# Kernel optimization log

Measured on AMD Instinct MI355X. Metric: run time of the kernel, lower is better.

Reference implementation:

```python
import jax, jax.numpy as jnp
import numpy as np

N_NODES = 100000
N_EDGES = 1600000
IN_DIM = 128
HID_DIM = 128
N_MASK = 5000
N_CLASSES = 4


def gcn_layer(x, src, dst, edge_weight, W, b):
    """PyG GCNConv: x' = D^{-1/2} (A + I) D^{-1/2} (x W) + b, with edge weights."""
    n = x.shape[0]
    loop = jnp.arange(n, dtype=src.dtype)
    s = jnp.concatenate([src, loop])                      # [E+N]
    d = jnp.concatenate([dst, loop])                      # [E+N]
    w = jnp.concatenate([edge_weight, jnp.ones((n,), edge_weight.dtype)])
    deg = jax.ops.segment_sum(w, d, num_segments=n)       # weighted in-degree incl. self-loop
    dis = jnp.where(deg > 0, jax.lax.rsqrt(deg), 0.0)     # deg^{-1/2}, inf -> 0
    norm = dis[s] * w * dis[d]                            # [E+N]
    h = x @ W                                             # [N, H] small GEMM
    msg = h[s] * norm[:, None]                            # gather + scale  [E+N, H]
    out = jax.ops.segment_sum(msg, d, num_segments=n)     # scatter-add     [N, H]
    return out + b


def setup_inputs() -> dict:
    key = jax.random.key(0)
    ks = jax.random.split(key, 8)
    x = jax.random.normal(ks[0], (N_NODES, IN_DIM), dtype=jnp.float32)
    edge_weight = jax.random.uniform(ks[1], (N_EDGES,), dtype=jnp.float32)
    W1 = jax.random.normal(ks[2], (IN_DIM, HID_DIM), dtype=jnp.float32) * (1.0 / np.sqrt(IN_DIM))
    b1 = jnp.zeros((HID_DIM,), jnp.float32)
    W2 = jax.random.normal(ks[3], (HID_DIM, HID_DIM), dtype=jnp.float32) * (1.0 / np.sqrt(HID_DIM))
    b2 = jnp.zeros((HID_DIM,), jnp.float32)
    edge_index = jax.random.randint(ks[4], (2, N_EDGES), 0, N_NODES, dtype=jnp.int32)
    mask_idx = jax.random.randint(ks[5], (N_MASK,), 0, N_NODES, dtype=jnp.int32)
    y = jax.random.randint(ks[6], (N_NODES,), 0, N_CLASSES, dtype=jnp.int32)
    return {"x": x, "edge_weight": edge_weight, "W1": W1, "b1": b1,
            "W2": W2, "b2": b2, "edge_index": edge_index,
            "mask_idx": mask_idx, "y": y}


def reference(x, edge_weight, W1, b1, W2, b2, edge_index, mask_idx, y):
    src, dst = edge_index[0], edge_index[1]
    h = gcn_layer(x, src, dst, edge_weight, W1, b1)
    h = jax.nn.relu(h)
    # F.dropout(training=False) in eval mode is identity
    h = gcn_layer(h, src, dst, edge_weight, W2, b2)
    return h[mask_idx], y[mask_idx]
```

## Files before the change

### kernel.cpp

```cpp
#include <hip/hip_runtime.h>

constexpr int N = 100000;
constexpr int E = 1600000;
constexpr int D = 128;
constexpr int M = 5000;

constexpr int MF_BLKS = (N + 255) / 256;

constexpr int NBITS = 7;
constexpr int BUCKET = 1 << NBITS;
constexpr int NB  = (N + BUCKET - 1) / BUCKET;
constexpr int EB  = 2048;
constexpr int NPB = (E + EB - 1) / EB;
constexpr int EBP = 8192;
constexpr int NPP = (E + EBP - 1) / EBP;
constexpr int PREP_BLKS = 32;
constexpr int MB_BLKS = (M + 255) / 256;

typedef __attribute__((ext_vector_type(8))) short bf16x8;
typedef __attribute__((ext_vector_type(4))) float f32x4;


__device__ __forceinline__ unsigned int pack_bf16x2(float a, float b) {
    unsigned int ua = __float_as_uint(a);
    unsigned int ub = __float_as_uint(b);
    ua = (ua + 0x7FFFu + ((ua >> 16) & 1u)) >> 16;
    ub = (ub + 0x7FFFu + ((ub >> 16) & 1u)) & 0xFFFF0000u;
    return ua | ub;
}
__device__ __forceinline__ unsigned short bf16_rne(float a) {
    unsigned int ua = __float_as_uint(a);
    return (unsigned short)((ua + 0x7FFFu + ((ua >> 16) & 1u)) >> 16);
}
__device__ __forceinline__ float bf16_lo(unsigned int u) { return __uint_as_float(u << 16); }
__device__ __forceinline__ float bf16_hi(unsigned int u) { return __uint_as_float(u & 0xFFFF0000u); }


__global__ __launch_bounds__(256) void k_misc1(const int* __restrict__ dst,
                                               int* __restrict__ bucketCnt,
                                               const float* __restrict__ W1,
                                               unsigned int* __restrict__ Wt1,
                                               const int* __restrict__ mask,
                                               unsigned int* __restrict__ maskbit,
                                               unsigned int* __restrict__ needed) {
    __shared__ int h[NB];
    const int t = threadIdx.x;
    if (blockIdx.x < NPB) {
        for (int i = t; i < NB; i += 256) h[i] = 0;
        __syncthreads();
        const int base = blockIdx.x * EB;
#pragma unroll
        for (int i = 0; i < 8; ++i) {
            int e = base + t + i * 256;
            if (e < E) {
                int b = __builtin_nontemporal_load(dst + e) >> NBITS;
                atomicAdd(&h[b], 1);
            }
        }
        __syncthreads();
        for (int i = t; i < NB; i += 256) {
            int c = h[i];
            if (c) atomicAdd(&bucketCnt[i], c);
        }
    } else if (blockIdx.x < NPB + PREP_BLKS) {
        int idx = (blockIdx.x - NPB) * 256 + t;
        int n = idx >> 6, kk = idx & 63;
        float a = W1[(2 * kk) * D + n];
        float b = W1[(2 * kk + 1) * D + n];
        Wt1[idx] = pack_bf16x2(a, b);
    } else {
        int i = (blockIdx.x - NPB - PREP_BLKS) * 256 + t;
        if (i < M) {
            int n = mask[i];
            atomicOr(&maskbit[n >> 5], 1u << (n & 31));
            atomicOr(&needed[n >> 5], 1u << (n & 31));
        }
    }
}


__global__ __launch_bounds__(256) void k_misc2(const int* __restrict__ bucketCnt,
                                               int* __restrict__ bucketBase,
                                               int* __restrict__ gCursor,
                                               const unsigned int* __restrict__ maskbit,
                                               const int* __restrict__ src,
                                               const int* __restrict__ dst,
                                               unsigned int* __restrict__ needed) {
    const int t = threadIdx.x;
    if (blockIdx.x == 0) {
        __shared__ int waveS[4];
        const int lane = t & 63, wave = t >> 6;
        const int idx = t * 4;
        int c[4];
        int s = 0;
#pragma unroll
        for (int g = 0; g < 4; ++g) {
            c[g] = (idx + g < NB) ? bucketCnt[idx + g] : 0;
            s += c[g];
        }
        int v = s;
        for (int off = 1; off < 64; off <<= 1) {
            int u = __shfl_up(v, off);
            if (lane >= off) v += u;
        }
        if (lane == 63) waveS[wave] = v;
        __syncthreads();
        int wb = 0;
        for (int w = 0; w < 4; ++w) if (w < wave) wb += waveS[w];
        int run = wb + v - s;
#pragma unroll
        for (int g = 0; g < 4; ++g) {
            int pos = idx + g;
            if (pos < NB) {
                bucketBase[pos] = run;
                gCursor[pos] = run;
            }
            run += c[g];
        }
        if (t == 255) bucketBase[NB] = E;
    } else {
        const int base = (blockIdx.x - 1) * EB;
#pragma unroll
        for (int i = 0; i < 8; ++i) {
            int e = base + t + i * 256;
            if (e < E) {
                int d = __builtin_nontemporal_load(dst + e);
                if ((maskbit[d >> 5] >> (d & 31)) & 1u) {
                    int s = src[e];
                    atomicOr(&needed[s >> 5], 1u << (s & 31));
                }
            }
        }
    }
}


__global__ __launch_bounds__(1024) void k_part(const int* __restrict__ src,
                                               const int* __restrict__ dst,
                                               const float* __restrict__ ew,
                                               int* __restrict__ gCursor,
                                               unsigned long long* __restrict__ tmp) {
    __shared__ int cnt[NB];
    __shared__ int off[NB];
    __shared__ int rk[NB];
    const int t = threadIdx.x;
    for (int i = t; i < NB; i += 1024) { cnt[i] = 0; rk[i] = 0; }
    __syncthreads();

    const int eb = blockIdx.x * EBP;
    int d_[8], s_[8];
    float w_[8];
#pragma unroll
    for (int i = 0; i < 8; ++i) {
        int e = eb + t + i * 1024;
        if (e < E) {
            d_[i] = __builtin_nontemporal_load(dst + e);
            s_[i] = __builtin_nontemporal_load(src + e);
            w_[i] = __builtin_nontemporal_load(ew + e);
            atomicAdd(&cnt[d_[i] >> NBITS], 1);
        } else {
            d_[i] = -1;
        }
    }
    __syncthreads();

    for (int i = t; i < NB; i += 1024) {
        int c = cnt[i];
        if (c > 0) off[i] = atomicAdd(&gCursor[i], c);
    }
    __syncthreads();

#pragma unroll
    for (int i = 0; i < 8; ++i) {
        if (d_[i] >= 0) {
            int b = d_[i] >> NBITS;
            int r = atomicAdd(&rk[b], 1);
            unsigned long long rec =
                ((unsigned long long)(unsigned int)__float_as_int(w_[i]) << 32) |
                ((unsigned int)s_[i] << NBITS) | (unsigned int)(d_[i] & (BUCKET - 1));
            tmp[(size_t)off[b] + r] = rec;
        }
    }
}


union SMem {
    unsigned int Ws[128 * 68];
    struct { int cnt[BUCKET]; float wsum[BUCKET]; int off[BUCKET]; int waveS[2]; } l;
};


template <bool BF16IN>
__device__ __forceinline__ void gemm_mfma_body(unsigned int* __restrict__ Ws,
                                               const void* __restrict__ Xin,
                                               const unsigned int* __restrict__ Wt,
                                               unsigned short* __restrict__ out, int blk) {
    const int t = threadIdx.x;
#pragma unroll
    for (int i = 0; i < 8; ++i) {
        int f4 = t + i * 256;
        int n = f4 >> 4;
        int k4 = f4 & 15;
        uint4 w = ((const uint4*)Wt)[f4];
        *(uint4*)(&Ws[n * 68 + k4 * 4]) = w;
    }
    __syncthreads();

    const int wv = t >> 6, lane = t & 63;
    const int q = lane >> 4, l15 = lane & 15;
    const int rowBase = blk * 256 + wv * 64;

    f32x4 acc[4][8] = {};
#pragma unroll
    for (int kc = 0; kc < 4; ++kc) {
        bf16x8 af[4];
#pragma unroll
        for (int rt = 0; rt < 4; ++rt) {
            int row = rowBase + rt * 16 + l15;
            if (row > N - 1) row = N - 1;
            union { uint4 u; bf16x8 v; } cv;
            if (BF16IN) {
                cv.u = *(const uint4*)((const unsigned int*)Xin + (size_t)row * 64 + kc * 16 + q * 4);
            } else {
                const float* xr = (const float*)Xin + (size_t)row * D + kc * 32 + q * 8;
                float4 x0 = *(const float4*)xr;
                float4 x1 = *(const float4*)(xr + 4);
                cv.u.x = pack_bf16x2(x0.x, x0.y);
                cv.u.y = pack_bf16x2(x0.z, x0.w);
                cv.u.z = pack_bf16x2(x1.x, x1.y);
                cv.u.w = pack_bf16x2(x1.z, x1.w);
            }
            af[rt] = cv.v;
        }
#pragma unroll
        for (int ct = 0; ct < 8; ++ct) {
            union { uint4 u; bf16x8 v; } bv;
            bv.u = *(const uint4*)(&Ws[(ct * 16 + l15) * 68 + kc * 16 + q * 4]);
#pragma unroll
            for (int rt = 0; rt < 4; ++rt)
                acc[rt][ct] = __builtin_amdgcn_mfma_f32_16x16x32_bf16(af[rt], bv.v, acc[rt][ct], 0, 0, 0);
        }
    }

#pragma unroll
    for (int rt = 0; rt < 4; ++rt) {
#pragma unroll
        for (int ct = 0; ct < 8; ++ct) {
            int col = ct * 16 + l15;
#pragma unroll
            for (int r = 0; r < 4; ++r) {
                int row = rowBase + rt * 16 + q * 4 + r;
                if (row < N) out[(size_t)row * D + col] = bf16_rne(acc[rt][ct][r]);
            }
        }
    }
}


__device__ __forceinline__ void local_a_body(SMem& sm,
                                             const unsigned long long* __restrict__ tmp,
                                             const int* __restrict__ bucketBase,
                                             float* __restrict__ dis,
                                             int* __restrict__ rowStart,
                                             int* __restrict__ offG) {
    const int b = blockIdx.x;
    const int t = threadIdx.x;
    const int segBeg = bucketBase[b];
    const int segEnd = bucketBase[b + 1];

    int*   cnt   = sm.l.cnt;
    float* wsum  = sm.l.wsum;
    int*   waveS = sm.l.waveS;
    if (t < BUCKET) { cnt[t] = 0; wsum[t] = 0.f; }
    __syncthreads();

    for (int e = segBeg + t; e < segEnd; e += 256) {
        unsigned long long rec = tmp[e];
        int dl = (int)(rec & (BUCKET - 1));
        float w = __uint_as_float((unsigned int)(rec >> 32));
        atomicAdd(&cnt[dl], 1);
        atomicAdd(&wsum[dl], w);
    }
    __syncthreads();

    const int lane = t & 63, wv = t >> 6;
    const int pv = (t < BUCKET) ? cnt[t] : 0;
    int v = pv;
    for (int o = 1; o < 64; o <<= 1) {
        int u = __shfl_up(v, o);
        if (lane >= o) v += u;
    }
    if (lane == 63 && wv < 2) waveS[wv] = v;
    __syncthreads();
    if (t < BUCKET) {
        const int wb = (wv == 1) ? waveS[0] : 0;
        const int ex = wb + v - pv;
        offG[b * BUCKET + t] = ex;
        const int node = b * BUCKET + t;
        if (node < N) { rowStart[node] = segBeg + ex; dis[node] = rsqrtf(1.0f + wsum[t]); }
    }
    if (b == NB - 1 && t == 0) rowStart[N] = E;
}


__global__ __launch_bounds__(256) void k_local_g1(const unsigned long long* __restrict__ tmp,
                                                  const int* __restrict__ bucketBase,
                                                  float* __restrict__ dis,
                                                  int* __restrict__ rowStart,
                                                  int* __restrict__ offG,
                                                  const float* __restrict__ x,
                                                  const unsigned int* __restrict__ Wt1,
                                                  unsigned short* __restrict__ A) {
    __shared__ SMem sm;
    if (blockIdx.x < NB) {
        local_a_body(sm, tmp, bucketBase, dis, rowStart, offG);
    } else {
        gemm_mfma_body<false>(sm.Ws, x, Wt1, A, blockIdx.x - NB);
    }
}


__global__ __launch_bounds__(256) void k_local_b(const unsigned long long* __restrict__ tmp,
                                                 const int* __restrict__ bucketBase,
                                                 const int* __restrict__ offG,
                                                 const float* __restrict__ dis,
                                                 int2* __restrict__ pairs) {
    __shared__ int cnt[BUCKET];
    __shared__ int off[BUCKET];
    const int b = blockIdx.x;
    const int t = threadIdx.x;
    if (t < BUCKET) { cnt[t] = 0; off[t] = offG[b * BUCKET + t]; }
    __syncthreads();
    const int segBeg = bucketBase[b];
    const int segEnd = bucketBase[b + 1];
    for (int e = segBeg + t; e < segEnd; e += 256) {
        unsigned long long rec = tmp[e];
        int dl = (int)(rec & (BUCKET - 1));
        int s  = (int)((rec >> NBITS) & 0xFFFFF);
        float w = __uint_as_float((unsigned int)(rec >> 32));
        float v = w * dis[s];
        int r = atomicAdd(&cnt[dl], 1);
        pairs[segBeg + off[dl] + r] = make_int2(s, __float_as_int(v));
    }
}


__global__ __launch_bounds__(256) void k_aggregate(const unsigned int* __restrict__ Hb,
                                                   const int2* __restrict__ pairs,
                                                   const int* __restrict__ rowStart,
                                                   const float* __restrict__ dis,
                                                   const unsigned int* __restrict__ needed,
                                                   const float* __restrict__ b,
                                                   unsigned int* __restrict__ outB) {
    int node = blockIdx.x * 4 + (threadIdx.x >> 6);
    if (node >= N) return;
    if (!((needed[node >> 5] >> (node & 31)) & 1u)) return;
    int lane = threadIdx.x & 63;
    int beg = rowStart[node], end = rowStart[node + 1];

    float ax = 0.f, ay = 0.f;
    int j = beg;
    for (; j + 7 < end; j += 8) {
        int2 p[8];
        unsigned int h[8];
#pragma unroll
        for (int i = 0; i < 8; ++i) p[i] = pairs[j + i];
#pragma unroll
        for (int i = 0; i < 8; ++i) h[i] = Hb[(size_t)p[i].x * 64 + lane];
#pragma unroll
        for (int i = 0; i < 8; ++i) {
            float v = __int_as_float(p[i].y);
            ax += bf16_lo(h[i]) * v;
            ay += bf16_hi(h[i]) * v;
        }
    }
    for (; j + 3 < end; j += 4) {
        int2 p[4];
        unsigned int h[4];
#pragma unroll
        for (int i = 0; i < 4; ++i) p[i] = pairs[j + i];
#pragma unroll
        for (int i = 0; i < 4; ++i) h[i] = Hb[(size_t)p[i].x * 64 + lane];
#pragma unroll
        for (int i = 0; i < 4; ++i) {
            float v = __int_as_float(p[i].y);
            ax += bf16_lo(h[i]) * v;
            ay += bf16_hi(h[i]) * v;
        }
    }
    for (; j < end; ++j) {
        int2 p0 = pairs[j];
        unsigned int h0 = Hb[(size_t)p0.x * 64 + lane];
        float v0 = __int_as_float(p0.y);
        ax += bf16_lo(h0) * v0;
        ay += bf16_hi(h0) * v0;
    }

    float dd = dis[node];
    float sn = dd * dd;
    unsigned int hs = Hb[(size_t)node * 64 + lane];
    float2 bb = ((const float2*)b)[lane];
    float ox = fmaxf(ax * dd + bf16_lo(hs) * sn + bb.x, 0.f);
    float oy = fmaxf(ay * dd + bf16_hi(hs) * sn + bb.y, 0.f);
    __builtin_nontemporal_store(pack_bf16x2(ox, oy), outB + (size_t)node * 64 + lane);
}


__global__ __launch_bounds__(256) void k_agg_mask_B(const unsigned int* __restrict__ Hb,
                                                    const int2* __restrict__ pairs,
                                                    const int* __restrict__ rowStart,
                                                    const float* __restrict__ dis,
                                                    const int* __restrict__ mask,
                                                    const int* __restrict__ y,
                                                    float* __restrict__ aggB,
                                                    float* __restrict__ out) {
    int i = blockIdx.x * 4 + (threadIdx.x >> 6);
    if (i >= M) return;
    int lane = threadIdx.x & 63;
    int node = mask[i];
    int beg = rowStart[node], end = rowStart[node + 1];

    float ax = 0.f, ay = 0.f;
    int j = beg;
    for (; j + 7 < end; j += 8) {
        int2 p[8];
        unsigned int h[8];
#pragma unroll
        for (int ii = 0; ii < 8; ++ii) p[ii] = pairs[j + ii];
#pragma unroll
        for (int ii = 0; ii < 8; ++ii) h[ii] = Hb[(size_t)p[ii].x * 64 + lane];
#pragma unroll
        for (int ii = 0; ii < 8; ++ii) {
            float v = __int_as_float(p[ii].y);
            ax += bf16_lo(h[ii]) * v;
            ay += bf16_hi(h[ii]) * v;
        }
    }
    for (; j < end; ++j) {
        int2 p0 = pairs[j];
        unsigned int h0 = Hb[(size_t)p0.x * 64 + lane];
        float v0 = __int_as_float(p0.y);
        ax += bf16_lo(h0) * v0;
        ay += bf16_hi(h0) * v0;
    }

    float dd = dis[node];
    float sn = dd * dd;
    unsigned int hs = Hb[(size_t)node * 64 + lane];
    float ox = ax * dd + bf16_lo(hs) * sn;
    float oy = ay * dd + bf16_hi(hs) * sn;
    ((float2*)(aggB + (size_t)i * D))[lane] = make_float2(ox, oy);
    if (lane == 0) out[(size_t)M * D + i] = (float)y[node];
}


__global__ __launch_bounds__(256) void k_out_gemm(const float* __restrict__ aggB,
                                                  const float* __restrict__ W2,
                                                  const float* __restrict__ b2,
                                                  float* __restrict__ out) {
    __shared__ float w2s[128 * 132];
    __shared__ float rowL[4][128];
    const int t = threadIdx.x;
    const int wv = t >> 6, lane = t & 63;
    const int row = blockIdx.x * 4 + wv;

    for (int i = t; i < 4096; i += 256) {
        float4 v = ((const float4*)W2)[i];
        int k = (4 * i) >> 7, n = (4 * i) & 127;
        *(float4*)(&w2s[k * 132 + n]) = v;
    }
    float2 a2 = ((const float2*)(aggB + (size_t)row * D))[lane];
    rowL[wv][2 * lane] = a2.x;
    rowL[wv][2 * lane + 1] = a2.y;
    __syncthreads();

    float2 bb = ((const float2*)b2)[lane];
    float acc0 = bb.x, acc1 = bb.y;
#pragma unroll 8
    for (int k = 0; k < 128; ++k) {
        float a = rowL[wv][k];
        float2 w = *(const float2*)(&w2s[k * 132 + 2 * lane]);
        acc0 += a * w.x;
        acc1 += a * w.y;
    }
    ((float2*)(out + (size_t)row * D))[lane] = make_float2(acc0, acc1);
}

extern "C" void kernel_launch(void* const* d_in, const int* in_sizes, int n_in,
                              void* d_out, int out_size, void* d_ws, size_t ws_size,
                              hipStream_t stream) {
    const float* x  = (const float*)d_in[0];
    const float* ew = (const float*)d_in[1];
    const float* W1 = (const float*)d_in[2];
    const float* b1 = (const float*)d_in[3];
    const float* W2 = (const float*)d_in[4];
    const float* b2 = (const float*)d_in[5];
    const int* eidx = (const int*)d_in[6];
    const int* mask = (const int*)d_in[7];
    const int* y    = (const int*)d_in[8];
    const int* src = eidx;
    const int* dst = eidx + E;

    char* ws = (char*)d_ws;
    float* dis      = (float*)(ws);
    int*   rowStart = (int*)(ws + (size_t)512 * 1024);
    unsigned int* maskbit = (unsigned int*)(ws + (size_t)960 * 1024);
    unsigned int* needed  = (unsigned int*)(ws + (size_t)976 * 1024);
    int*   bucketCnt  = (int*)(ws + (size_t)992 * 1024);
    int*   bucketBase = (int*)(ws + (size_t)996 * 1024);
    int*   gCursor    = (int*)(ws + (size_t)1000 * 1024);
    unsigned int* Wt1 = (unsigned int*)(ws + (size_t)1008 * 1024);
    int*   offG     = (int*)(ws + (size_t)1040 * 1024);
    int2*  pairs    = (int2*)(ws + (size_t)2 * 1024 * 1024);
    unsigned long long* tmp = (unsigned long long*)(ws + (size_t)16 * 1024 * 1024);
    unsigned short* A  = (unsigned short*)(ws + (size_t)29 * 1024 * 1024);
    unsigned short* B  = (unsigned short*)(ws + (size_t)55 * 1024 * 1024);
    float* aggB = (float*)(ws + (size_t)81 * 1024 * 1024);

    (void)hipMemsetAsync(ws + (size_t)960 * 1024, 0, (size_t)40 * 1024, stream);
    hipLaunchKernelGGL(k_misc1, dim3(NPB + PREP_BLKS + MB_BLKS), dim3(256), 0, stream,
                       dst, bucketCnt, W1, Wt1, mask, maskbit, needed);

    hipLaunchKernelGGL(k_misc2, dim3(1 + NPB), dim3(256), 0, stream,
                       bucketCnt, bucketBase, gCursor, maskbit, src, dst, needed);

    hipLaunchKernelGGL(k_part, dim3(NPP), dim3(1024), 0, stream,
                       src, dst, ew, gCursor, tmp);

    hipLaunchKernelGGL(k_local_g1, dim3(NB + MF_BLKS), dim3(256), 0, stream,
                       tmp, bucketBase, dis, rowStart, offG, x, Wt1, A);

    hipLaunchKernelGGL(k_local_b, dim3(NB), dim3(256), 0, stream,
                       tmp, bucketBase, offG, dis, pairs);

    hipLaunchKernelGGL(k_aggregate, dim3((N + 3) / 4), dim3(256), 0, stream,
                       (const unsigned int*)A, pairs, rowStart, dis, needed, b1,
                       (unsigned int*)B);

    hipLaunchKernelGGL(k_agg_mask_B, dim3((M + 3) / 4), dim3(256), 0, stream,
                       (const unsigned int*)B, pairs, rowStart, dis, mask, y,
                       aggB, (float*)d_out);
    hipLaunchKernelGGL(k_out_gemm, dim3(M / 4), dim3(256), 0, stream,
                       aggB, W2, b2, (float*)d_out);
}
```

Measured before the change: 287.2 us.

## Fuse bucket-local sort with layer-1 aggregation and mask gather with output GEMM

Merges the per-bucket CSR scatter kernel with the layer-1 aggregation. Each 512-thread block sorts its bucket's edges into shared memory (when the bucket holds at most 3072 edges) and then aggregates its 128 nodes straight from LDS. This avoids re-reading pairs from global memory and drops one launch. The masked second-layer gather is also fused with the W2 GEMM, loading W2 in two halves to limit LDS, which removes the aggB round trip and another launch. The trade-offs are less parallelism in layer-1 aggregation (one block per 128 nodes instead of one wave per node), larger shared memory use, and a reload of W2 in every output block.

After: 276.0 us. 3.9% less time.

```diff
diff --git a/kernel.cpp b/kernel.cpp
--- a/kernel.cpp
+++ b/kernel.cpp
@@ -16,6 +16,7 @@
 constexpr int NPP = (E + EBP - 1) / EBP;
 constexpr int PREP_BLKS = 32;
 constexpr int MB_BLKS = (M + 255) / 256;
+constexpr int CAP = 3072;
 
 typedef __attribute__((ext_vector_type(8))) short bf16x8;
 typedef __attribute__((ext_vector_type(4))) float f32x4;
@@ -186,7 +187,7 @@
 
 union SMem {
     unsigned int Ws[128 * 68];
-    struct { int cnt[BUCKET]; float wsum[BUCKET]; int off[BUCKET]; int waveS[2]; } l;
+    struct { int cnt[BUCKET]; float wsum[BUCKET]; int waveS[2]; } l;
 };
 
 
@@ -261,7 +262,6 @@
                                              const unsigned long long* __restrict__ tmp,
                                              const int* __restrict__ bucketBase,
                                              float* __restrict__ dis,
-                                             int* __restrict__ rowStart,
                                              int* __restrict__ offG) {
     const int b = blockIdx.x;
     const int t = threadIdx.x;
@@ -297,66 +297,154 @@
         const int ex = wb + v - pv;
         offG[b * BUCKET + t] = ex;
         const int node = b * BUCKET + t;
-        if (node < N) { rowStart[node] = segBeg + ex; dis[node] = rsqrtf(1.0f + wsum[t]); }
-    }
-    if (b == NB - 1 && t == 0) rowStart[N] = E;
+        if (node < N) dis[node] = rsqrtf(1.0f + wsum[t]);
+    }
 }
 
 
 __global__ __launch_bounds__(256) void k_local_g1(const unsigned long long* __restrict__ tmp,
                                                   const int* __restrict__ bucketBase,
                                                   float* __restrict__ dis,
-                                                  int* __restrict__ rowStart,
                                                   int* __restrict__ offG,
                                                   const float* __restrict__ x,
                                                   const unsigned int* __restrict__ Wt1,
                                                   unsigned short* __restrict__ A) {
     __shared__ SMem sm;
     if (blockIdx.x < NB) {
-        local_a_body(sm, tmp, bucketBase, dis, rowStart, offG);
+        local_a_body(sm, tmp, bucketBase, dis, offG);
     } else {
         gemm_mfma_body<false>(sm.Ws, x, Wt1, A, blockIdx.x - NB);
     }
 }
 
 
-__global__ __launch_bounds__(256) void k_local_b(const unsigned long long* __restrict__ tmp,
-                                                 const int* __restrict__ bucketBase,
-                                                 const int* __restrict__ offG,
-                                                 const float* __restrict__ dis,
-                                                 int2* __restrict__ pairs) {
+__global__ __launch_bounds__(512) void k_sort_agg(const unsigned long long* __restrict__ tmp,
+                                                  const int* __restrict__ bucketBase,
+                                                  const int* __restrict__ offG,
+                                                  const float* __restrict__ dis,
+                                                  const unsigned int* __restrict__ needed,
+                                                  const float* __restrict__ b,
+                                                  const unsigned int* __restrict__ Hb,
+                                                  int* __restrict__ rowStart,
+                                                  int2* __restrict__ pairs,
+                                                  unsigned int* __restrict__ outB) {
+    __shared__ int2 lp[CAP];
     __shared__ int cnt[BUCKET];
-    __shared__ int off[BUCKET];
-    const int b = blockIdx.x;
-    const int t = threadIdx.x;
-    if (t < BUCKET) { cnt[t] = 0; off[t] = offG[b * BUCKET + t]; }
-    __syncthreads();
-    const int segBeg = bucketBase[b];
-    const int segEnd = bucketBase[b + 1];
-    for (int e = segBeg + t; e < segEnd; e += 256) {
+    __shared__ int offL[BUCKET + 1];
+    const int bk = blockIdx.x;
+    const int t = threadIdx.x;
+    const int segBeg = bucketBase[bk];
+    const int segEnd = bucketBase[bk + 1];
+    const int segLen = segEnd - segBeg;
+    const bool fits = (segLen <= CAP);
+
+    if (t < BUCKET) {
+        int ex = offG[bk * BUCKET + t];
+        offL[t] = ex;
+        cnt[t] = 0;
+        int node = bk * BUCKET + t;
+        if (node < N) rowStart[node] = segBeg + ex;
+    }
+    if (t == 0) offL[BUCKET] = segLen;
+    if (bk == NB - 1 && t == 0) rowStart[N] = E;
+    __syncthreads();
+
+    for (int e = segBeg + t; e < segEnd; e += 512) {
         unsigned long long rec = tmp[e];
         int dl = (int)(rec & (BUCKET - 1));
         int s  = (int)((rec >> NBITS) & 0xFFFFF);
         float w = __uint_as_float((unsigned int)(rec >> 32));
         float v = w * dis[s];
         int r = atomicAdd(&cnt[dl], 1);
-        pairs[segBeg + off[dl] + r] = make_int2(s, __float_as_int(v));
-    }
-}
-
-
-__global__ __launch_bounds__(256) void k_aggregate(const unsigned int* __restrict__ Hb,
-                                                   const int2* __restrict__ pairs,
-                                                   const int* __restrict__ rowStart,
-                                                   const float* __restrict__ dis,
-                                                   const unsigned int* __restrict__ needed,
-                                                   const float* __restrict__ b,
-                                                   unsigned int* __restrict__ outB) {
-    int node = blockIdx.x * 4 + (threadIdx.x >> 6);
-    if (node >= N) return;
-    if (!((needed[node >> 5] >> (node & 31)) & 1u)) return;
-    int lane = threadIdx.x & 63;
-    int beg = rowStart[node], end = rowStart[node + 1];
+        int pos = offL[dl] + r;
+        int2 pr = make_int2(s, __float_as_int(v));
+        pairs[segBeg + pos] = pr;
+        if (fits) lp[pos] = pr;
+    }
+    __syncthreads();
+
+    const int wv = t >> 6, lane = t & 63;
+    for (int k = 0; k < 16; ++k) {
+        const int nl = wv * 16 + k;
+        const int node = bk * BUCKET + nl;
+        if (node >= N) break;
+        if (!((needed[node >> 5] >> (node & 31)) & 1u)) continue;
+        const int beg = offL[nl], end = offL[nl + 1];
+        float ax = 0.f, ay = 0.f;
+        int j = beg;
+        if (fits) {
+            for (; j + 7 < end; j += 8) {
+                int2 p[8];
+                unsigned int h[8];
+#pragma unroll
+                for (int i = 0; i < 8; ++i) p[i] = lp[j + i];
+#pragma unroll
+                for (int i = 0; i < 8; ++i) h[i] = Hb[(size_t)p[i].x * 64 + lane];
+#pragma unroll
+                for (int i = 0; i < 8; ++i) {
+                    float v = __int_as_float(p[i].y);
+                    ax += bf16_lo(h[i]) * v;
+                    ay += bf16_hi(h[i]) * v;
+                }
+            }
+            for (; j < end; ++j) {
+                int2 p0 = lp[j];
+                unsigned int h0 = Hb[(size_t)p0.x * 64 + lane];
+                float v0 = __int_as_float(p0.y);
+                ax += bf16_lo(h0) * v0;
+                ay += bf16_hi(h0) * v0;
+            }
+        } else {
+            const int2* gp = pairs + segBeg;
+            for (; j + 7 < end; j += 8) {
+                int2 p[8];
+                unsigned int h[8];
+#pragma unroll
+                for (int i = 0; i < 8; ++i) p[i] = gp[j + i];
+#pragma unroll
+                for (int i = 0; i < 8; ++i) h[i] = Hb[(size_t)p[i].x * 64 + lane];
+#pragma unroll
+                for (int i = 0; i < 8; ++i) {
+                    float v = __int_as_float(p[i].y);
+                    ax += bf16_lo(h[i]) * v;
+                    ay += bf16_hi(h[i]) * v;
+                }
+            }
+            for (; j < end; ++j) {
+                int2 p0 = gp[j];
+                unsigned int h0 = Hb[(size_t)p0.x * 64 + lane];
+                float v0 = __int_as_float(p0.y);
+                ax += bf16_lo(h0) * v0;
+                ay += bf16_hi(h0) * v0;
+            }
+        }
+        float dd = dis[node];
+        float sn = dd * dd;
+        unsigned int hs = Hb[(size_t)node * 64 + lane];
+        float2 bb = ((const float2*)b)[lane];
+        float ox = fmaxf(ax * dd + bf16_lo(hs) * sn + bb.x, 0.f);
+        float oy = fmaxf(ay * dd + bf16_hi(hs) * sn + bb.y, 0.f);
+        __builtin_nontemporal_store(pack_bf16x2(ox, oy), outB + (size_t)node * 64 + lane);
+    }
+}
+
+
+__global__ __launch_bounds__(256) void k_mask_out(const unsigned int* __restrict__ Hb,
+                                                  const int2* __restrict__ pairs,
+                                                  const int* __restrict__ rowStart,
+                                                  const float* __restrict__ dis,
+                                                  const float* __restrict__ W2,
+                                                  const float* __restrict__ b2,
+                                                  const int* __restrict__ mask,
+                                                  const int* __restrict__ y,
+                                                  float* __restrict__ out) {
+    __shared__ float w2s[64 * 132];
+    __shared__ float rowL[4][128];
+    const int t = threadIdx.x;
+    const int wv = t >> 6, lane = t & 63;
+    const int i = blockIdx.x * 4 + wv;
+    const int node = mask[i];
+    const int beg = rowStart[node], end = rowStart[node + 1];
 
     float ax = 0.f, ay = 0.f;
     int j = beg;
@@ -364,28 +452,14 @@
         int2 p[8];
         unsigned int h[8];
 #pragma unroll
-        for (int i = 0; i < 8; ++i) p[i] = pairs[j + i];
-#pragma unroll
-        for (int i = 0; i < 8; ++i) h[i] = Hb[(size_t)p[i].x * 64 + lane];
-#pragma unroll
-        for (int i = 0; i < 8; ++i) {
-            float v = __int_as_float(p[i].y);
-            ax += bf16_lo(h[i]) * v;
-            ay += bf16_hi(h[i]) * v;
-        }
-    }
-    for (; j + 3 < end; j += 4) {
-        int2 p[4];
-        unsigned int h[4];
-#pragma unroll
-        for (int i = 0; i < 4; ++i) p[i] = pairs[j + i];
-#pragma unroll
-        for (int i = 0; i < 4; ++i) h[i] = Hb[(size_t)p[i].x * 64 + lane];
-#pragma unroll
-        for (int i = 0; i < 4; ++i) {
-            float v = __int_as_float(p[i].y);
-            ax += bf16_lo(h[i]) * v;
-            ay += bf16_hi(h[i]) * v;
+        for (int ii = 0; ii < 8; ++ii) p[ii] = pairs[j + ii];
+#pragma unroll
+        for (int ii = 0; ii < 8; ++ii) h[ii] = Hb[(size_t)p[ii].x * 64 + lane];
+#pragma unroll
+        for (int ii = 0; ii < 8; ++ii) {
+            float v = __int_as_float(p[ii].y);
+            ax += bf16_lo(h[ii]) * v;
+            ay += bf16_hi(h[ii]) * v;
         }
     }
     for (; j < end; ++j) {
@@ -395,95 +469,35 @@
         ax += bf16_lo(h0) * v0;
         ay += bf16_hi(h0) * v0;
     }
-
-    float dd = dis[node];
-    float sn = dd * dd;
-    unsigned int hs = Hb[(size_t)node * 64 + lane];
-    float2 bb = ((const float2*)b)[lane];
-    float ox = fmaxf(ax * dd + bf16_lo(hs) * sn + bb.x, 0.f);
-    float oy = fmaxf(ay * dd + bf16_hi(hs) * sn + bb.y, 0.f);
-    __builtin_nontemporal_store(pack_bf16x2(ox, oy), outB + (size_t)node * 64 + lane);
-}
-
-
-__global__ __launch_bounds__(256) void k_agg_mask_B(const unsigned int* __restrict__ Hb,
-                                                    const int2* __restrict__ pairs,
-                                                    const int* __restrict__ rowStart,
-                                                    const float* __restrict__ dis,
-                                                    const int* __restrict__ mask,
-                                                    const int* __restrict__ y,
-                                                    float* __restrict__ aggB,
-                                                    float* __restrict__ out) {
-    int i = blockIdx.x * 4 + (threadIdx.x >> 6);
-    if (i >= M) return;
-    int lane = threadIdx.x & 63;
-    int node = mask[i];
-    int beg = rowStart[node], end = rowStart[node + 1];
-
-    float ax = 0.f, ay = 0.f;
-    int j = beg;
-    for (; j + 7 < end; j += 8) {
-        int2 p[8];
-        unsigned int h[8];
-#pragma unroll
-        for (int ii = 0; ii < 8; ++ii) p[ii] = pairs[j + ii];
-#pragma unroll
-        for (int ii = 0; ii < 8; ++ii) h[ii] = Hb[(size_t)p[ii].x * 64 + lane];
-#pragma unroll
-        for (int ii = 0; ii < 8; ++ii) {
-            float v = __int_as_float(p[ii].y);
-            ax += bf16_lo(h[ii]) * v;
-            ay += bf16_hi(h[ii]) * v;
-        }
-    }
-    for (; j < end; ++j) {
-        int2 p0 = pairs[j];
-        unsigned int h0 = Hb[(size_t)p0.x * 64 + lane];
-        float v0 = __int_as_float(p0.y);
-        ax += bf16_lo(h0) * v0;
-        ay += bf16_hi(h0) * v0;
-    }
-
-    float dd = dis[node];
-    float sn = dd * dd;
-    unsigned int hs = Hb[(size_t)node * 64 + lane];
-    float ox = ax * dd + bf16_lo(hs) * sn;
-    float oy = ay * dd + bf16_hi(hs) * sn;
-    ((float2*)(aggB + (size_t)i * D))[lane] = make_float2(ox, oy);
-    if (lane == 0) out[(size_t)M * D + i] = (float)y[node];
-}
-
-
-__global__ __launch_bounds__(256) void k_out_gemm(const float* __restrict__ aggB,
-                                                  const float* __restrict__ W2,
-                                                  const float* __restrict__ b2,
-                                                  float* __restrict__ out) {
-    __shared__ float w2s[128 * 132];
-    __shared__ float rowL[4][128];
-    const int t = threadIdx.x;
-    const int wv = t >> 6, lane = t & 63;
-    const int row = blockIdx.x * 4 + wv;
-
-    for (int i = t; i < 4096; i += 256) {
-        float4 v = ((const float4*)W2)[i];
-        int k = (4 * i) >> 7, n = (4 * i) & 127;
-        *(float4*)(&w2s[k * 132 + n]) = v;
-    }
-    float2 a2 = ((const float2*)(aggB + (size_t)row * D))[lane];
-    rowL[wv][2 * lane] = a2.x;
-    rowL[wv][2 * lane + 1] = a2.y;
-    __syncthreads();
+    {
+        float dd = dis[node];
+        float sn = dd * dd;
+        unsigned int hs = Hb[(size_t)node * 64 + lane];
+        rowL[wv][2 * lane]     = ax * dd + bf16_lo(hs) * sn;
+        rowL[wv][2 * lane + 1] = ay * dd + bf16_hi(hs) * sn;
+    }
 
     float2 bb = ((const float2*)b2)[lane];
     float acc0 = bb.x, acc1 = bb.y;
+#pragma unroll
+    for (int h0 = 0; h0 < 2; ++h0) {
+        __syncthreads();
+        for (int idx = t; idx < 2048; idx += 256) {
+            float4 v = ((const float4*)W2)[h0 * 2048 + idx];
+            int k = (idx * 4) >> 7, n = (idx * 4) & 127;
+            *(float4*)(&w2s[k * 132 + n]) = v;
+        }
+        __syncthreads();
 #pragma unroll 8
-    for (int k = 0; k < 128; ++k) {
-        float a = rowL[wv][k];
-        float2 w = *(const float2*)(&w2s[k * 132 + 2 * lane]);
-        acc0 += a * w.x;
-        acc1 += a * w.y;
-    }
-    ((float2*)(out + (size_t)row * D))[lane] = make_float2(acc0, acc1);
+        for (int k = 0; k < 64; ++k) {
+            float a = rowL[wv][h0 * 64 + k];
+            float2 w = *(const float2*)(&w2s[k * 132 + 2 * lane]);
+            acc0 += a * w.x;
+            acc1 += a * w.y;
+        }
+    }
+    ((float2*)(out + (size_t)i * D))[lane] = make_float2(acc0, acc1);
+    if (lane == 0) out[(size_t)M * D + i] = (float)y[node];
 }
 
 extern "C" void kernel_launch(void* const* d_in, const int* in_sizes, int n_in,
@@ -515,7 +529,6 @@
     unsigned long long* tmp = (unsigned long long*)(ws + (size_t)16 * 1024 * 1024);
     unsigned short* A  = (unsigned short*)(ws + (size_t)29 * 1024 * 1024);
     unsigned short* B  = (unsigned short*)(ws + (size_t)55 * 1024 * 1024);
-    float* aggB = (float*)(ws + (size_t)81 * 1024 * 1024);
 
     (void)hipMemsetAsync(ws + (size_t)960 * 1024, 0, (size_t)40 * 1024, stream);
     hipLaunchKernelGGL(k_misc1, dim3(NPB + PREP_BLKS + MB_BLKS), dim3(256), 0, stream,
@@ -528,18 +541,13 @@
                        src, dst, ew, gCursor, tmp);
 
     hipLaunchKernelGGL(k_local_g1, dim3(NB + MF_BLKS), dim3(256), 0, stream,
-                       tmp, bucketBase, dis, rowStart, offG, x, Wt1, A);
-
-    hipLaunchKernelGGL(k_local_b, dim3(NB), dim3(256), 0, stream,
-                       tmp, bucketBase, offG, dis, pairs);
-
-    hipLaunchKernelGGL(k_aggregate, dim3((N + 3) / 4), dim3(256), 0, stream,
-                       (const unsigned int*)A, pairs, rowStart, dis, needed, b1,
-                       (unsigned int*)B);
-
-    hipLaunchKernelGGL(k_agg_mask_B, dim3((M + 3) / 4), dim3(256), 0, stream,
-                       (const unsigned int*)B, pairs, rowStart, dis, mask, y,
-                       aggB, (float*)d_out);
-    hipLaunchKernelGGL(k_out_gemm, dim3(M / 4), dim3(256), 0, stream,
-                       aggB, W2, b2, (float*)d_out);
-}
+                       tmp, bucketBase, dis, offG, x, Wt1, A);
+
+    hipLaunchKernelGGL(k_sort_agg, dim3(NB), dim3(512), 0, stream,
+                       tmp, bucketBase, offG, dis, needed, b1,
+                       (const unsigned int*)A, rowStart, pairs, (unsigned int*)B);
+
+    hipLaunchKernelGGL(k_mask_out, dim3(M / 4), dim3(256), 0, stream,
+                       (const unsigned int*)B, pairs, rowStart, dis, W2, b2,
+                       mask, y, (float*)d_out);
+}
```
